# Optimization experiments

Hardware: AMD Instinct MI355X
Metric: run time of the kernel (lower is better)

Reference implementation:

```python
import jax, jax.numpy as jnp
import numpy as np

N_NODES = 100000
N_EDGES = 1000000
D_IN, D_HID, D_OUT = 20, 64, 64
NEG_SLOPE = 0.2


def _gat_layer(x, src, dst, W, a_src, a_dst, b, n_nodes):
    """PyG-style single-head GATConv: message j->i, softmax over incoming edges of i."""
    h = x @ W                                  # [N, D]
    alpha_s = h @ a_src                        # [N]
    alpha_d = h @ a_dst                        # [N]
    e = jax.nn.leaky_relu(alpha_s[src] + alpha_d[dst], NEG_SLOPE)  # [E]
    # numerically-stable segment softmax over destination nodes
    m = jax.ops.segment_max(e, dst, num_segments=n_nodes)          # [N]
    ex = jnp.exp(e - m[dst])                                       # [E]
    denom = jax.ops.segment_sum(ex, dst, num_segments=n_nodes)     # [N]
    alpha = ex / denom[dst]                                        # [E]
    out = jax.ops.segment_sum(alpha[:, None] * h[src], dst, num_segments=n_nodes)
    return out + b


def setup_inputs() -> dict:
    key = jax.random.key(0)
    ks = jax.random.split(key, 11)
    x = jax.random.normal(ks[0], (N_NODES, D_IN), dtype=jnp.float32)
    edge_index = jax.random.randint(ks[1], (2, N_EDGES), 0, N_NODES, dtype=jnp.int64)
    s1 = 1.0 / np.sqrt(D_IN)
    s2 = 1.0 / np.sqrt(D_HID)
    return {
        "x": x,
        "edge_index": edge_index,
        "W1": jax.random.normal(ks[2], (D_IN, D_HID), dtype=jnp.float32) * s1,
        "a_src1": jax.random.normal(ks[3], (D_HID,), dtype=jnp.float32) * s2,
        "a_dst1": jax.random.normal(ks[4], (D_HID,), dtype=jnp.float32) * s2,
        "b1": jnp.zeros((D_HID,), dtype=jnp.float32),
        "W2": jax.random.normal(ks[5], (D_HID, D_OUT), dtype=jnp.float32) * s2,
        "a_src2": jax.random.normal(ks[6], (D_OUT,), dtype=jnp.float32) * s2,
        "a_dst2": jax.random.normal(ks[7], (D_OUT,), dtype=jnp.float32) * s2,
        "b2": jnp.zeros((D_OUT,), dtype=jnp.float32),
    }


def reference(x, edge_index, W1, a_src1, a_dst1, b1, W2, a_src2, a_dst2, b2):
    n = x.shape[0]
    # PyG GATConv adds self-loops by default
    loops = jnp.arange(n, dtype=edge_index.dtype)
    src = jnp.concatenate([edge_index[0], loops])
    dst = jnp.concatenate([edge_index[1], loops])
    h = _gat_layer(x, src, dst, W1, a_src1, a_dst1, b1, n)
    h = jax.nn.relu(h)
    # dropout(p=0.2) is identity in eval mode
    h = _gat_layer(h, src, dst, W2, a_src2, a_dst2, b2, n)
    # global_mean_pool with all-zero batch -> mean over all nodes, shape [1, D_OUT]
    return jnp.mean(h, axis=0, keepdims=True)
```

## Files before the change

### kernel.cpp

```cpp
#include <hip/hip_runtime.h>
#include <math.h>

#define NDIM 64
#define LRELU_SLOPE 0.2f
#define BSHIFT 8
#define BNODES 256
#define ECAP 3584
#define CCAP (ECAP + BNODES)

typedef float f32x2 __attribute__((ext_vector_type(2)));

__device__ __forceinline__ ushort f2bf(float f) {
    unsigned u = __float_as_uint(f);
    unsigned r = (u + 0x7fffu + ((u >> 16) & 1u)) >> 16;
    return (ushort)r;
}
__device__ __forceinline__ float bflo(unsigned u) { return __uint_as_float(u << 16); }
__device__ __forceinline__ float bfhi(unsigned u) { return __uint_as_float(u & 0xffff0000u); }

__global__ void initb_kernel(int* __restrict__ bcur, int nb) {
    int i = blockIdx.x * blockDim.x + threadIdx.x;
    if (i < nb) bcur[i] = i * ECAP;
}

__global__ __launch_bounds__(256) void pg_kernel(
    const int* __restrict__ src, const int* __restrict__ dst,
    int* __restrict__ bcur, unsigned* __restrict__ part, int E, int nb, int PB,
    const float* __restrict__ X, const float* __restrict__ W,
    const float* __restrict__ asrc, const float* __restrict__ adst,
    unsigned char* __restrict__ h, float* __restrict__ as_,
    float* __restrict__ ad_, int N) {
    int t = threadIdx.x;
    if ((int)blockIdx.x < PB) {
        __shared__ int hist[512];
        __shared__ int base[512];
        for (int i = t; i < nb; i += 256) hist[i] = 0;
        __syncthreads();
        int chunk = blockIdx.x * 4096;
        int s[16], d[16];
#pragma unroll
        for (int j = 0; j < 4; ++j) {
            int idx = chunk + j * 1024 + t * 4;
            if (idx + 3 < E) {
                int4 sv = *(const int4*)(src + idx);
                int4 dv = *(const int4*)(dst + idx);
                s[j*4+0]=sv.x; s[j*4+1]=sv.y; s[j*4+2]=sv.z; s[j*4+3]=sv.w;
                d[j*4+0]=dv.x; d[j*4+1]=dv.y; d[j*4+2]=dv.z; d[j*4+3]=dv.w;
            } else {
#pragma unroll
                for (int q = 0; q < 4; ++q) {
                    int i2 = idx + q;
                    if (i2 < E) { s[j*4+q] = src[i2]; d[j*4+q] = dst[i2]; }
                    else        { s[j*4+q] = 0;       d[j*4+q] = -1; }
                }
            }
        }
#pragma unroll
        for (int j = 0; j < 16; ++j)
            if (d[j] >= 0) atomicAdd(&hist[d[j] >> BSHIFT], 1);
        __syncthreads();
        for (int i = t; i < nb; i += 256) {
            int c = hist[i];
            base[i] = c ? atomicAdd(&bcur[i], c) : 0;
            hist[i] = 0;
        }
        __syncthreads();
#pragma unroll
        for (int j = 0; j < 16; ++j) {
            if (d[j] >= 0) {
                int b = d[j] >> BSHIFT;
                int pos = base[b] + atomicAdd(&hist[b], 1);
                int lim = (b + 1) * ECAP - 1;
                if (pos > lim) pos = lim;
                part[pos] = ((unsigned)(d[j] & (BNODES - 1)) << 17) | (unsigned)s[j];
            }
        }
    } else {
        const int K = 20, KS = 32;
        __shared__ float xs[64 * 32];
        __shared__ unsigned hsq[64 * 17];
        __shared__ float ps[2][4][64];
        int base2 = (blockIdx.x - PB) * 64;
        for (int i = t; i < 64 * KS; i += 256) {
            int nl = i / KS, k = i - nl * KS;
            int node = base2 + nl;
            float v = (k < K && node < N) ? X[(size_t)node * K + k] : 0.f;
            xs[nl * KS + ((k + nl) & (KS - 1))] = v;
        }
        __syncthreads();
        int wid = __builtin_amdgcn_readfirstlane(t >> 6);
        int lane = t & 63;
        int node = base2 + lane;
        float acc[16];
#pragma unroll
        for (int j = 0; j < 16; ++j) acc[j] = 0.f;
        const float* Wg = W + wid * 16;
        const float* xrow = xs + lane * KS;
#pragma unroll 4
        for (int k = 0; k < K; ++k) {
            float xk = xrow[(k + lane) & (KS - 1)];
#pragma unroll
            for (int j = 0; j < 16; ++j)
                acc[j] = fmaf(xk, Wg[k * 64 + j], acc[j]);
        }
        float s = 0.f, d = 0.f;
#pragma unroll
        for (int j = 0; j < 16; ++j) {
            s = fmaf(acc[j], asrc[wid * 16 + j], s);
            d = fmaf(acc[j], adst[wid * 16 + j], d);
        }
        ps[0][wid][lane] = s;
        ps[1][wid][lane] = d;
#pragma unroll
        for (int j = 0; j < 16; j += 4) {
            int q = (wid * 16 + j) >> 2;
            int sp = (q + lane) & 15;
            int u = __builtin_amdgcn_cvt_pk_fp8_f32(acc[j], acc[j + 1], 0, false);
            u = __builtin_amdgcn_cvt_pk_fp8_f32(acc[j + 2], acc[j + 3], u, true);
            hsq[lane * 17 + sp] = (unsigned)u;
        }
        __syncthreads();
        if (wid == 0) {
            float s4 = ps[0][0][lane] + ps[0][1][lane] + ps[0][2][lane] + ps[0][3][lane];
            float d4 = ps[1][0][lane] + ps[1][1][lane] + ps[1][2][lane] + ps[1][3][lane];
            if (node < N) { as_[node] = s4; ad_[node] = d4; }
        }
        unsigned* hout = (unsigned*)h;
        for (int pass = 0; pass < 4; ++pass) {
            int row = pass * 16 + (t >> 4);
            int q = t & 15;
            int sp = (q + row) & 15;
            unsigned v = hsq[row * 17 + sp];
            int n2 = base2 + row;
            if (n2 < N) hout[(size_t)n2 * 16 + q] = v;
        }
    }
}

__global__ __launch_bounds__(256) void csr_kernel(
    const int* __restrict__ bcur, const unsigned* __restrict__ part,
    int* __restrict__ csr, int2* __restrict__ offlen, int N) {
    __shared__ int hist[256];
    __shared__ int sc[256];
    int b = blockIdx.x, t = threadIdx.x;
    int nodeBase = b << BSHIFT;
    int nNodes = min(BNODES, N - nodeBase);
    int count = min(bcur[b] - b * ECAP, ECAP);
    hist[t] = (t < nNodes) ? 1 : 0;
    __syncthreads();
    const unsigned* slice = part + (size_t)b * ECAP;
    for (int i = t; i < count; i += 256) {
        int dl = (int)(slice[i] >> 17);
        atomicAdd(&hist[dl], 1);
    }
    __syncthreads();
    int cnt = hist[t];
    sc[t] = cnt;
    __syncthreads();
    for (int o = 1; o < 256; o <<= 1) {
        int v = sc[t];
        int u = (t >= o) ? sc[t - o] : 0;
        __syncthreads();
        sc[t] = v + u;
        __syncthreads();
    }
    int excl = sc[t] - cnt;
    int boff = b * CCAP;
    if (t < nNodes) {
        offlen[nodeBase + t] = make_int2(boff + excl, cnt);
        csr[boff + excl] = nodeBase + t;
    }
    hist[t] = excl + 1;
    __syncthreads();
    for (int i = t; i < count; i += 256) {
        unsigned e = slice[i];
        int dl = (int)(e >> 17);
        int pos = boff + atomicAdd(&hist[dl], 1);
        csr[pos] = (int)(e & 0x1ffffu);
    }
}

template<int K, int KS, bool BF16IN>
__global__ __launch_bounds__(256) void gemm_kernel(
    const void* __restrict__ Xv, const float* __restrict__ W,
    const float* __restrict__ asrc, const float* __restrict__ adst,
    unsigned char* __restrict__ h, float* __restrict__ as_, float* __restrict__ ad_, int N) {
    __shared__ float xs[64 * KS];
    __shared__ unsigned hsq[64 * 17];
    __shared__ float ps[2][4][64];
    int t = threadIdx.x;
    int base = blockIdx.x * 64;
    if (BF16IN) {
        const unsigned* X = (const unsigned*)Xv;
        for (int i = t; i < 64 * (K / 2); i += 256) {
            int nl = i / (K / 2), p = i - nl * (K / 2);
            int k = p * 2;
            int node = base + nl;
            unsigned u = (node < N) ? X[(size_t)node * (K / 2) + p] : 0u;
            xs[nl * KS + ((k + nl) & (KS - 1))] = bflo(u);
            xs[nl * KS + ((k + 1 + nl) & (KS - 1))] = bfhi(u);
        }
    } else {
        const float* X = (const float*)Xv;
        for (int i = t; i < 64 * KS; i += 256) {
            int nl = i / KS, k = i - nl * KS;
            int node = base + nl;
            float v = (k < K && node < N) ? X[(size_t)node * K + k] : 0.f;
            xs[nl * KS + ((k + nl) & (KS - 1))] = v;
        }
    }
    __syncthreads();
    int wid = __builtin_amdgcn_readfirstlane(t >> 6);
    int lane = t & 63;
    int node = base + lane;
    float acc[16];
#pragma unroll
    for (int j = 0; j < 16; ++j) acc[j] = 0.f;
    const float* Wg = W + wid * 16;
    const float* xrow = xs + lane * KS;
#pragma unroll 4
    for (int k = 0; k < K; ++k) {
        float xk = xrow[(k + lane) & (KS - 1)];
#pragma unroll
        for (int j = 0; j < 16; ++j)
            acc[j] = fmaf(xk, Wg[k * 64 + j], acc[j]);
    }
    float s = 0.f, d = 0.f;
#pragma unroll
    for (int j = 0; j < 16; ++j) {
        s = fmaf(acc[j], asrc[wid * 16 + j], s);
        d = fmaf(acc[j], adst[wid * 16 + j], d);
    }
    ps[0][wid][lane] = s;
    ps[1][wid][lane] = d;
#pragma unroll
    for (int j = 0; j < 16; j += 4) {
        int q = (wid * 16 + j) >> 2;
        int sp = (q + lane) & 15;
        int u = __builtin_amdgcn_cvt_pk_fp8_f32(acc[j], acc[j + 1], 0, false);
        u = __builtin_amdgcn_cvt_pk_fp8_f32(acc[j + 2], acc[j + 3], u, true);
        hsq[lane * 17 + sp] = (unsigned)u;
    }
    __syncthreads();
    if (wid == 0) {
        float s4 = ps[0][0][lane] + ps[0][1][lane] + ps[0][2][lane] + ps[0][3][lane];
        float d4 = ps[1][0][lane] + ps[1][1][lane] + ps[1][2][lane] + ps[1][3][lane];
        if (node < N) { as_[node] = s4; ad_[node] = d4; }
    }
    unsigned* hout = (unsigned*)h;
    for (int pass = 0; pass < 4; ++pass) {
        int row = pass * 16 + (t >> 4);
        int q = t & 15;
        int sp = (q + row) & 15;
        unsigned v = hsq[row * 17 + sp];
        int n2 = base + row;
        if (n2 < N) hout[(size_t)n2 * 16 + q] = v;
    }
}

__global__ __launch_bounds__(256) void agg_kernel(
    const int2* __restrict__ offlen, const int* __restrict__ csr,
    const float* __restrict__ as_, const float* __restrict__ ad_,
    const unsigned char* __restrict__ hsrc, const float* __restrict__ bias,
    ushort* __restrict__ out, float* __restrict__ pool, int n, int mode) {
    __shared__ float psum[8][NDIM];
    int wid = threadIdx.x >> 6, lane = threadIdx.x & 63;
    int half = lane >> 5;
    int lh = lane & 31;
    int g = lh >> 3;
    int l = lane & 7;
    int hw = wid * 2 + half;
    int node = blockIdx.x * 8 + hw;
    int base_lane = lane & 32;
    float v[8];
#pragma unroll
    for (int j = 0; j < 8; ++j) v[j] = 0.f;
    if (node < n) {
        int2 ol = offlen[node];
        int off = ol.x, len = ol.y;
        float adi = ad_[node];
        bool vpre = lh < len;
        int skpre = vpre ? csr[off + lh] : 0;
        float apre = vpre ? as_[skpre] : 0.f;
        float tpre = apre + adi;
        tpre = (tpre > 0.f) ? tpre : LRELU_SLOPE * tpre;
        float expre = vpre ? __expf(tpre) : 0.f;
        float den = expre;
        den += __shfl_xor(den, 1);
        den += __shfl_xor(den, 2);
        den += __shfl_xor(den, 4);
        den += __shfl_xor(den, 8);
        den += __shfl_xor(den, 16);
        float acc[8];
#pragma unroll
        for (int j = 0; j < 8; ++j) acc[j] = 0.f;
        if (__all(len <= 32)) {
            uint2 hv[8];
            float exs[8];
#pragma unroll
            for (int c = 0; c < 8; ++c) {
                int e = c * 4 + g;
                int sk = __shfl(skpre, base_lane + e);
                exs[c] = __shfl(expre, base_lane + e);
                const uint2* p = (const uint2*)(hsrc + ((size_t)sk << 6) + (l << 3));
                hv[c] = (e < len) ? *p : make_uint2(0u, 0u);
            }
#pragma unroll
            for (int c = 0; c < 8; ++c) {
                float ex = exs[c];
                f32x2 p0 = __builtin_amdgcn_cvt_pk_f32_fp8(hv[c].x, false);
                f32x2 p1 = __builtin_amdgcn_cvt_pk_f32_fp8(hv[c].x, true);
                f32x2 p2 = __builtin_amdgcn_cvt_pk_f32_fp8(hv[c].y, false);
                f32x2 p3 = __builtin_amdgcn_cvt_pk_f32_fp8(hv[c].y, true);
                acc[0] = fmaf(ex, p0.x, acc[0]);
                acc[1] = fmaf(ex, p0.y, acc[1]);
                acc[2] = fmaf(ex, p1.x, acc[2]);
                acc[3] = fmaf(ex, p1.y, acc[3]);
                acc[4] = fmaf(ex, p2.x, acc[4]);
                acc[5] = fmaf(ex, p2.y, acc[5]);
                acc[6] = fmaf(ex, p3.x, acc[6]);
                acc[7] = fmaf(ex, p3.y, acc[7]);
            }
        } else {
            float den_tail = 0.f;
            int niter = (len + 3) >> 2;
            int sk0 = __shfl(skpre, base_lane + g);
            float ex0 = __shfl(expre, base_lane + g);
            bool ve0 = g < len;
            uint2 hv0 = make_uint2(0, 0);
            if (ve0) hv0 = *(const uint2*)(hsrc + ((size_t)sk0 << 6) + (l << 3));
            int sk1 = __shfl(skpre, base_lane + 4 + g);
            float ex1 = __shfl(expre, base_lane + 4 + g);
            bool ve1 = (4 + g) < len;
            uint2 hv1 = make_uint2(0, 0);
            if (ve1) hv1 = *(const uint2*)(hsrc + ((size_t)sk1 << 6) + (l << 3));
            for (int i = 0; i < niter; ++i) {
                float ex = ex0;
                uint2 hv = hv0;
                ex0 = ex1; hv0 = hv1;
                int e2 = (i + 2) * 4 + g;
                bool ve2 = e2 < len;
                int esrc = e2 < 32 ? e2 : 31;
                sk1 = __shfl(skpre, base_lane + esrc);
                ex1 = __shfl(expre, base_lane + esrc);
                if (e2 >= 32) {
                    if (ve2) {
                        sk1 = csr[off + e2];
                        float a = as_[sk1];
                        float tt = a + adi;
                        tt = (tt > 0.f) ? tt : LRELU_SLOPE * tt;
                        ex1 = __expf(tt);
                        den_tail += ex1;
                    } else ex1 = 0.f;
                }
                hv1 = make_uint2(0, 0);
                if (ve2) hv1 = *(const uint2*)(hsrc + ((size_t)sk1 << 6) + (l << 3));
                f32x2 p0 = __builtin_amdgcn_cvt_pk_f32_fp8(hv.x, false);
                f32x2 p1 = __builtin_amdgcn_cvt_pk_f32_fp8(hv.x, true);
                f32x2 p2 = __builtin_amdgcn_cvt_pk_f32_fp8(hv.y, false);
                f32x2 p3 = __builtin_amdgcn_cvt_pk_f32_fp8(hv.y, true);
                acc[0] = fmaf(ex, p0.x, acc[0]);
                acc[1] = fmaf(ex, p0.y, acc[1]);
                acc[2] = fmaf(ex, p1.x, acc[2]);
                acc[3] = fmaf(ex, p1.y, acc[3]);
                acc[4] = fmaf(ex, p2.x, acc[4]);
                acc[5] = fmaf(ex, p2.y, acc[5]);
                acc[6] = fmaf(ex, p3.x, acc[6]);
                acc[7] = fmaf(ex, p3.y, acc[7]);
            }
            den_tail += __shfl_xor(den_tail, 8);
            den_tail += __shfl_xor(den_tail, 16);
            den += den_tail;
        }
#pragma unroll
        for (int j = 0; j < 8; ++j) {
            acc[j] += __shfl_xor(acc[j], 8);
            acc[j] += __shfl_xor(acc[j], 16);
        }
        float inv = 1.f / den;
        const float4 bv0 = *(const float4*)(bias + l * 8);
        const float4 bv1 = *(const float4*)(bias + l * 8 + 4);
        v[0] = fmaf(acc[0], inv, bv0.x);
        v[1] = fmaf(acc[1], inv, bv0.y);
        v[2] = fmaf(acc[2], inv, bv0.z);
        v[3] = fmaf(acc[3], inv, bv0.w);
        v[4] = fmaf(acc[4], inv, bv1.x);
        v[5] = fmaf(acc[5], inv, bv1.y);
        v[6] = fmaf(acc[6], inv, bv1.z);
        v[7] = fmaf(acc[7], inv, bv1.w);
        if (mode == 1) {
#pragma unroll
            for (int j = 0; j < 8; ++j) v[j] = fmaxf(v[j], 0.f);
            if (g == 0) {
                uint4 pk;
                pk.x = (unsigned)f2bf(v[0]) | ((unsigned)f2bf(v[1]) << 16);
                pk.y = (unsigned)f2bf(v[2]) | ((unsigned)f2bf(v[3]) << 16);
                pk.z = (unsigned)f2bf(v[4]) | ((unsigned)f2bf(v[5]) << 16);
                pk.w = (unsigned)f2bf(v[6]) | ((unsigned)f2bf(v[7]) << 16);
                *(uint4*)(out + (size_t)node * NDIM + l * 8) = pk;
            }
        }
    }
    if (mode == 2) {
        if (g == 0) {
#pragma unroll
            for (int j = 0; j < 8; ++j) psum[hw][l * 8 + j] = v[j];
        }
        __syncthreads();
        if (threadIdx.x < NDIM) {
            float t = 0.f;
#pragma unroll
            for (int r = 0; r < 8; ++r) t += psum[r][threadIdx.x];
            pool[(size_t)blockIdx.x * NDIM + threadIdx.x] = t;
        }
    }
}

__global__ void mean_kernel(const float* __restrict__ pool, float* __restrict__ out,
                            int nb, float invn) {
    __shared__ float sm[4][NDIM];
    int lane = threadIdx.x & 63, wid = threadIdx.x >> 6;
    int row = blockIdx.x * 4 + wid;
    int stride = gridDim.x * 4;
    float s = 0.f;
    for (int i = row; i < nb; i += stride) s += pool[(long)i * NDIM + lane];
    sm[wid][lane] = s;
    __syncthreads();
    if (wid == 0) {
        float v = sm[0][lane] + sm[1][lane] + sm[2][lane] + sm[3][lane];
        atomicAdd(&out[lane], v * invn);
    }
}

extern "C" void kernel_launch(void* const* d_in, const int* in_sizes, int n_in,
                              void* d_out, int out_size, void* d_ws, size_t ws_size,
                              hipStream_t stream) {
    const float* x      = (const float*)d_in[0];
    const int*   eidx   = (const int*)d_in[1];
    const float* W1     = (const float*)d_in[2];
    const float* a_src1 = (const float*)d_in[3];
    const float* a_dst1 = (const float*)d_in[4];
    const float* b1     = (const float*)d_in[5];
    const float* W2     = (const float*)d_in[6];
    const float* a_src2 = (const float*)d_in[7];
    const float* a_dst2 = (const float*)d_in[8];
    const float* b2     = (const float*)d_in[9];
    float* out = (float*)d_out;

    const int N = in_sizes[0] / 20;
    const int E = in_sizes[1] / 2;
    const int* src = eidx;
    const int* dst = eidx + E;
    const int NB = (N + BNODES - 1) >> BSHIFT;

    const int gemm_blocks = (N + 63) / 64;
    const int agg_blocks  = (N + 7) / 8;
    const int PB = (E + 4095) / 4096;

    char* ws = (char*)d_ws;
    unsigned char* h = (unsigned char*)ws;
    ushort* o   = (ushort*)(h + (size_t)N * NDIM);
    float* as_  = (float*)(o + (size_t)N * NDIM);
    float* ad_  = as_ + N;
    int2*  offlen = (int2*)(ad_ + N);
    int*   csr  = (int*)(offlen + N);
    float* pool = (float*)(csr + (size_t)NB * CCAP);
    int*   bcur = (int*)(pool + (size_t)agg_blocks * NDIM);
    unsigned* part = (unsigned*)(bcur + NB);

    hipMemsetAsync(d_out, 0, (size_t)out_size * sizeof(float), stream);

    initb_kernel<<<(NB + 255) / 256, 256, 0, stream>>>(bcur, NB);
    pg_kernel<<<PB + gemm_blocks, 256, 0, stream>>>(
        src, dst, bcur, part, E, NB, PB,
        x, W1, a_src1, a_dst1, h, as_, ad_, N);
    csr_kernel<<<NB, 256, 0, stream>>>(bcur, part, csr, offlen, N);

    agg_kernel<<<agg_blocks, 256, 0, stream>>>(offlen, csr, as_, ad_, h, b1, o, pool, N, 1);

    gemm_kernel<64, 64, true><<<gemm_blocks, 256, 0, stream>>>(o, W2, a_src2, a_dst2, h, as_, ad_, N);
    agg_kernel<<<agg_blocks, 256, 0, stream>>>(offlen, csr, as_, ad_, h, b2, o, pool, N, 2);

    mean_kernel<<<64, 256, 0, stream>>>(pool, out, agg_blocks, 1.0f / (float)N);
}
```

Before: 196.4 us.

## Fuse all GAT stages into one persistent cooperative kernel with grid syncs

Replaces the six separate launches (bucket init, partition plus first GEMM, CSR build, two aggregations, second GEMM, mean) with one persistent cooperative kernel. Each block loops over work units of every stage, and grid-wide barriers separate the stages. Pooling now accumulates per block in shared memory and ends with one atomic per block instead of writing a pool buffer that a separate mean kernel reduces. This removes launch gaps and the pool round-trip, at the cost of grid.sync overhead, a grid capped by occupancy, and register pressure from the union of all stages.

```diff
diff --git a/kernel.cpp b/kernel.cpp
--- a/kernel.cpp
+++ b/kernel.cpp
@@ -1,5 +1,8 @@
 #include <hip/hip_runtime.h>
+#include <hip/hip_cooperative_groups.h>
 #include <math.h>
+
+namespace cg = cooperative_groups;
 
 #define NDIM 64
 #define LRELU_SLOPE 0.2f
@@ -18,178 +21,69 @@
 __device__ __forceinline__ float bflo(unsigned u) { return __uint_as_float(u << 16); }
 __device__ __forceinline__ float bfhi(unsigned u) { return __uint_as_float(u & 0xffff0000u); }
 
-__global__ void initb_kernel(int* __restrict__ bcur, int nb) {
-    int i = blockIdx.x * blockDim.x + threadIdx.x;
-    if (i < nb) bcur[i] = i * ECAP;
-}
-
-__global__ __launch_bounds__(256) void pg_kernel(
+#define SMEM_BYTES 22784
+
+__device__ __forceinline__ void part_unit(
+    unsigned char* SMEM, int unit,
     const int* __restrict__ src, const int* __restrict__ dst,
-    int* __restrict__ bcur, unsigned* __restrict__ part, int E, int nb, int PB,
-    const float* __restrict__ X, const float* __restrict__ W,
+    int* __restrict__ bcur, unsigned* __restrict__ part, int E, int nb) {
+    int* hist = (int*)SMEM;
+    int* base = (int*)(SMEM + 2048);
+    int t = threadIdx.x;
+    for (int i = t; i < nb; i += 256) hist[i] = 0;
+    __syncthreads();
+    int chunk = unit * 4096;
+    int s[16], d[16];
+#pragma unroll
+    for (int j = 0; j < 4; ++j) {
+        int idx = chunk + j * 1024 + t * 4;
+        if (idx + 3 < E) {
+            int4 sv = *(const int4*)(src + idx);
+            int4 dv = *(const int4*)(dst + idx);
+            s[j*4+0]=sv.x; s[j*4+1]=sv.y; s[j*4+2]=sv.z; s[j*4+3]=sv.w;
+            d[j*4+0]=dv.x; d[j*4+1]=dv.y; d[j*4+2]=dv.z; d[j*4+3]=dv.w;
+        } else {
+#pragma unroll
+            for (int q = 0; q < 4; ++q) {
+                int i2 = idx + q;
+                if (i2 < E) { s[j*4+q] = src[i2]; d[j*4+q] = dst[i2]; }
+                else        { s[j*4+q] = 0;       d[j*4+q] = -1; }
+            }
+        }
+    }
+#pragma unroll
+    for (int j = 0; j < 16; ++j)
+        if (d[j] >= 0) atomicAdd(&hist[d[j] >> BSHIFT], 1);
+    __syncthreads();
+    for (int i = t; i < nb; i += 256) {
+        int c = hist[i];
+        base[i] = c ? atomicAdd(&bcur[i], c) : 0;
+        hist[i] = 0;
+    }
+    __syncthreads();
+#pragma unroll
+    for (int j = 0; j < 16; ++j) {
+        if (d[j] >= 0) {
+            int b = d[j] >> BSHIFT;
+            int pos = base[b] + atomicAdd(&hist[b], 1);
+            int lim = (b + 1) * ECAP - 1;
+            if (pos > lim) pos = lim;
+            part[pos] = ((unsigned)(d[j] & (BNODES - 1)) << 17) | (unsigned)s[j];
+        }
+    }
+}
+
+template<int K, int KS, bool BF16IN>
+__device__ __forceinline__ void gemm_unit(
+    unsigned char* SMEM, int base,
+    const void* __restrict__ Xv, const float* __restrict__ W,
     const float* __restrict__ asrc, const float* __restrict__ adst,
     unsigned char* __restrict__ h, float* __restrict__ as_,
     float* __restrict__ ad_, int N) {
+    float* xs = (float*)SMEM;
+    unsigned* hsq = (unsigned*)(SMEM + 16384);
+    auto ps = (float(*)[4][64])(SMEM + 20736);
     int t = threadIdx.x;
-    if ((int)blockIdx.x < PB) {
-        __shared__ int hist[512];
-        __shared__ int base[512];
-        for (int i = t; i < nb; i += 256) hist[i] = 0;
-        __syncthreads();
-        int chunk = blockIdx.x * 4096;
-        int s[16], d[16];
-#pragma unroll
-        for (int j = 0; j < 4; ++j) {
-            int idx = chunk + j * 1024 + t * 4;
-            if (idx + 3 < E) {
-                int4 sv = *(const int4*)(src + idx);
-                int4 dv = *(const int4*)(dst + idx);
-                s[j*4+0]=sv.x; s[j*4+1]=sv.y; s[j*4+2]=sv.z; s[j*4+3]=sv.w;
-                d[j*4+0]=dv.x; d[j*4+1]=dv.y; d[j*4+2]=dv.z; d[j*4+3]=dv.w;
-            } else {
-#pragma unroll
-                for (int q = 0; q < 4; ++q) {
-                    int i2 = idx + q;
-                    if (i2 < E) { s[j*4+q] = src[i2]; d[j*4+q] = dst[i2]; }
-                    else        { s[j*4+q] = 0;       d[j*4+q] = -1; }
-                }
-            }
-        }
-#pragma unroll
-        for (int j = 0; j < 16; ++j)
-            if (d[j] >= 0) atomicAdd(&hist[d[j] >> BSHIFT], 1);
-        __syncthreads();
-        for (int i = t; i < nb; i += 256) {
-            int c = hist[i];
-            base[i] = c ? atomicAdd(&bcur[i], c) : 0;
-            hist[i] = 0;
-        }
-        __syncthreads();
-#pragma unroll
-        for (int j = 0; j < 16; ++j) {
-            if (d[j] >= 0) {
-                int b = d[j] >> BSHIFT;
-                int pos = base[b] + atomicAdd(&hist[b], 1);
-                int lim = (b + 1) * ECAP - 1;
-                if (pos > lim) pos = lim;
-                part[pos] = ((unsigned)(d[j] & (BNODES - 1)) << 17) | (unsigned)s[j];
-            }
-        }
-    } else {
-        const int K = 20, KS = 32;
-        __shared__ float xs[64 * 32];
-        __shared__ unsigned hsq[64 * 17];
-        __shared__ float ps[2][4][64];
-        int base2 = (blockIdx.x - PB) * 64;
-        for (int i = t; i < 64 * KS; i += 256) {
-            int nl = i / KS, k = i - nl * KS;
-            int node = base2 + nl;
-            float v = (k < K && node < N) ? X[(size_t)node * K + k] : 0.f;
-            xs[nl * KS + ((k + nl) & (KS - 1))] = v;
-        }
-        __syncthreads();
-        int wid = __builtin_amdgcn_readfirstlane(t >> 6);
-        int lane = t & 63;
-        int node = base2 + lane;
-        float acc[16];
-#pragma unroll
-        for (int j = 0; j < 16; ++j) acc[j] = 0.f;
-        const float* Wg = W + wid * 16;
-        const float* xrow = xs + lane * KS;
-#pragma unroll 4
-        for (int k = 0; k < K; ++k) {
-            float xk = xrow[(k + lane) & (KS - 1)];
-#pragma unroll
-            for (int j = 0; j < 16; ++j)
-                acc[j] = fmaf(xk, Wg[k * 64 + j], acc[j]);
-        }
-        float s = 0.f, d = 0.f;
-#pragma unroll
-        for (int j = 0; j < 16; ++j) {
-            s = fmaf(acc[j], asrc[wid * 16 + j], s);
-            d = fmaf(acc[j], adst[wid * 16 + j], d);
-        }
-        ps[0][wid][lane] = s;
-        ps[1][wid][lane] = d;
-#pragma unroll
-        for (int j = 0; j < 16; j += 4) {
-            int q = (wid * 16 + j) >> 2;
-            int sp = (q + lane) & 15;
-            int u = __builtin_amdgcn_cvt_pk_fp8_f32(acc[j], acc[j + 1], 0, false);
-            u = __builtin_amdgcn_cvt_pk_fp8_f32(acc[j + 2], acc[j + 3], u, true);
-            hsq[lane * 17 + sp] = (unsigned)u;
-        }
-        __syncthreads();
-        if (wid == 0) {
-            float s4 = ps[0][0][lane] + ps[0][1][lane] + ps[0][2][lane] + ps[0][3][lane];
-            float d4 = ps[1][0][lane] + ps[1][1][lane] + ps[1][2][lane] + ps[1][3][lane];
-            if (node < N) { as_[node] = s4; ad_[node] = d4; }
-        }
-        unsigned* hout = (unsigned*)h;
-        for (int pass = 0; pass < 4; ++pass) {
-            int row = pass * 16 + (t >> 4);
-            int q = t & 15;
-            int sp = (q + row) & 15;
-            unsigned v = hsq[row * 17 + sp];
-            int n2 = base2 + row;
-            if (n2 < N) hout[(size_t)n2 * 16 + q] = v;
-        }
-    }
-}
-
-__global__ __launch_bounds__(256) void csr_kernel(
-    const int* __restrict__ bcur, const unsigned* __restrict__ part,
-    int* __restrict__ csr, int2* __restrict__ offlen, int N) {
-    __shared__ int hist[256];
-    __shared__ int sc[256];
-    int b = blockIdx.x, t = threadIdx.x;
-    int nodeBase = b << BSHIFT;
-    int nNodes = min(BNODES, N - nodeBase);
-    int count = min(bcur[b] - b * ECAP, ECAP);
-    hist[t] = (t < nNodes) ? 1 : 0;
-    __syncthreads();
-    const unsigned* slice = part + (size_t)b * ECAP;
-    for (int i = t; i < count; i += 256) {
-        int dl = (int)(slice[i] >> 17);
-        atomicAdd(&hist[dl], 1);
-    }
-    __syncthreads();
-    int cnt = hist[t];
-    sc[t] = cnt;
-    __syncthreads();
-    for (int o = 1; o < 256; o <<= 1) {
-        int v = sc[t];
-        int u = (t >= o) ? sc[t - o] : 0;
-        __syncthreads();
-        sc[t] = v + u;
-        __syncthreads();
-    }
-    int excl = sc[t] - cnt;
-    int boff = b * CCAP;
-    if (t < nNodes) {
-        offlen[nodeBase + t] = make_int2(boff + excl, cnt);
-        csr[boff + excl] = nodeBase + t;
-    }
-    hist[t] = excl + 1;
-    __syncthreads();
-    for (int i = t; i < count; i += 256) {
-        unsigned e = slice[i];
-        int dl = (int)(e >> 17);
-        int pos = boff + atomicAdd(&hist[dl], 1);
-        csr[pos] = (int)(e & 0x1ffffu);
-    }
-}
-
-template<int K, int KS, bool BF16IN>
-__global__ __launch_bounds__(256) void gemm_kernel(
-    const void* __restrict__ Xv, const float* __restrict__ W,
-    const float* __restrict__ asrc, const float* __restrict__ adst,
-    unsigned char* __restrict__ h, float* __restrict__ as_, float* __restrict__ ad_, int N) {
-    __shared__ float xs[64 * KS];
-    __shared__ unsigned hsq[64 * 17];
-    __shared__ float ps[2][4][64];
-    int t = threadIdx.x;
-    int base = blockIdx.x * 64;
     if (BF16IN) {
         const unsigned* X = (const unsigned*)Xv;
         for (int i = t; i < 64 * (K / 2); i += 256) {
@@ -258,19 +152,64 @@
     }
 }
 
-__global__ __launch_bounds__(256) void agg_kernel(
+__device__ __forceinline__ void csr_unit(
+    unsigned char* SMEM, int b,
+    const int* __restrict__ bcur, const unsigned* __restrict__ part,
+    int* __restrict__ csr, int2* __restrict__ offlen, int N) {
+    int* hist = (int*)SMEM;
+    int* sc = (int*)(SMEM + 1024);
+    int t = threadIdx.x;
+    int nodeBase = b << BSHIFT;
+    int nNodes = min(BNODES, N - nodeBase);
+    int count = min(bcur[b] - b * ECAP, ECAP);
+    hist[t] = (t < nNodes) ? 1 : 0;
+    __syncthreads();
+    const unsigned* slice = part + (size_t)b * ECAP;
+    for (int i = t; i < count; i += 256) {
+        int dl = (int)(slice[i] >> 17);
+        atomicAdd(&hist[dl], 1);
+    }
+    __syncthreads();
+    int cnt = hist[t];
+    sc[t] = cnt;
+    __syncthreads();
+    for (int o = 1; o < 256; o <<= 1) {
+        int v = sc[t];
+        int u = (t >= o) ? sc[t - o] : 0;
+        __syncthreads();
+        sc[t] = v + u;
+        __syncthreads();
+    }
+    int excl = sc[t] - cnt;
+    int boff = b * CCAP;
+    if (t < nNodes) {
+        offlen[nodeBase + t] = make_int2(boff + excl, cnt);
+        csr[boff + excl] = nodeBase + t;
+    }
+    hist[t] = excl + 1;
+    __syncthreads();
+    for (int i = t; i < count; i += 256) {
+        unsigned e = slice[i];
+        int dl = (int)(e >> 17);
+        int pos = boff + atomicAdd(&hist[dl], 1);
+        csr[pos] = (int)(e & 0x1ffffu);
+    }
+}
+
+template<int MODE>
+__device__ __forceinline__ void agg_unit(
+    unsigned char* SMEM, int unit,
     const int2* __restrict__ offlen, const int* __restrict__ csr,
     const float* __restrict__ as_, const float* __restrict__ ad_,
     const unsigned char* __restrict__ hsrc, const float* __restrict__ bias,
-    ushort* __restrict__ out, float* __restrict__ pool, int n, int mode) {
-    __shared__ float psum[8][NDIM];
+    ushort* __restrict__ out_, float* __restrict__ bacc, int n) {
     int wid = threadIdx.x >> 6, lane = threadIdx.x & 63;
     int half = lane >> 5;
     int lh = lane & 31;
     int g = lh >> 3;
     int l = lane & 7;
     int hw = wid * 2 + half;
-    int node = blockIdx.x * 8 + hw;
+    int node = unit * 8 + hw;
     int base_lane = lane & 32;
     float v[8];
 #pragma unroll
@@ -388,7 +327,7 @@
         v[5] = fmaf(acc[5], inv, bv1.y);
         v[6] = fmaf(acc[6], inv, bv1.z);
         v[7] = fmaf(acc[7], inv, bv1.w);
-        if (mode == 1) {
+        if (MODE == 1) {
 #pragma unroll
             for (int j = 0; j < 8; ++j) v[j] = fmaxf(v[j], 0.f);
             if (g == 0) {
@@ -397,38 +336,80 @@
                 pk.y = (unsigned)f2bf(v[2]) | ((unsigned)f2bf(v[3]) << 16);
                 pk.z = (unsigned)f2bf(v[4]) | ((unsigned)f2bf(v[5]) << 16);
                 pk.w = (unsigned)f2bf(v[6]) | ((unsigned)f2bf(v[7]) << 16);
-                *(uint4*)(out + (size_t)node * NDIM + l * 8) = pk;
+                *(uint4*)(out_ + (size_t)node * NDIM + l * 8) = pk;
             }
         }
     }
-    if (mode == 2) {
+    if (MODE == 2) {
+        auto psum = (float(*)[NDIM])SMEM;
         if (g == 0) {
 #pragma unroll
             for (int j = 0; j < 8; ++j) psum[hw][l * 8 + j] = v[j];
         }
         __syncthreads();
         if (threadIdx.x < NDIM) {
-            float t = 0.f;
-#pragma unroll
-            for (int r = 0; r < 8; ++r) t += psum[r][threadIdx.x];
-            pool[(size_t)blockIdx.x * NDIM + threadIdx.x] = t;
-        }
-    }
-}
-
-__global__ void mean_kernel(const float* __restrict__ pool, float* __restrict__ out,
-                            int nb, float invn) {
-    __shared__ float sm[4][NDIM];
-    int lane = threadIdx.x & 63, wid = threadIdx.x >> 6;
-    int row = blockIdx.x * 4 + wid;
-    int stride = gridDim.x * 4;
-    float s = 0.f;
-    for (int i = row; i < nb; i += stride) s += pool[(long)i * NDIM + lane];
-    sm[wid][lane] = s;
-    __syncthreads();
-    if (wid == 0) {
-        float v = sm[0][lane] + sm[1][lane] + sm[2][lane] + sm[3][lane];
-        atomicAdd(&out[lane], v * invn);
+            float s = 0.f;
+#pragma unroll
+            for (int r = 0; r < 8; ++r) s += psum[r][threadIdx.x];
+            bacc[threadIdx.x] += s;
+        }
+        __syncthreads();
+    }
+}
+
+__global__ __launch_bounds__(256, 4) void giga_kernel(
+    const int* __restrict__ src, const int* __restrict__ dst,
+    int* __restrict__ bcur, unsigned* __restrict__ part,
+    int E, int nb, int PB, int GB, int AU,
+    const float* __restrict__ x,
+    const float* __restrict__ W1, const float* __restrict__ as1v,
+    const float* __restrict__ ad1v, const float* __restrict__ b1,
+    const float* __restrict__ W2, const float* __restrict__ as2v,
+    const float* __restrict__ ad2v, const float* __restrict__ b2,
+    unsigned char* __restrict__ h, ushort* __restrict__ o,
+    float* __restrict__ as_, float* __restrict__ ad_,
+    int2* __restrict__ offlen, int* __restrict__ csr,
+    float* __restrict__ out, int N, float invn) {
+    __shared__ __align__(16) unsigned char SMEM[SMEM_BYTES];
+    cg::grid_group grid = cg::this_grid();
+    int t = threadIdx.x;
+    int G = gridDim.x;
+
+    for (int i = blockIdx.x * 256 + t; i < nb; i += G * 256) bcur[i] = i * ECAP;
+    grid.sync();
+
+    for (int u = blockIdx.x; u < PB + GB; u += G) {
+        if (u < PB) part_unit(SMEM, u, src, dst, bcur, part, E, nb);
+        else gemm_unit<20, 32, false>(SMEM, (u - PB) * 64, x, W1, as1v, ad1v, h, as_, ad_, N);
+        __syncthreads();
+    }
+    grid.sync();
+
+    for (int u = blockIdx.x; u < nb; u += G) {
+        csr_unit(SMEM, u, bcur, part, csr, offlen, N);
+        __syncthreads();
+    }
+    grid.sync();
+
+    for (int u = blockIdx.x; u < AU; u += G)
+        agg_unit<1>(SMEM, u, offlen, csr, as_, ad_, h, b1, o, nullptr, N);
+    grid.sync();
+
+    for (int u = blockIdx.x; u < GB; u += G) {
+        gemm_unit<64, 64, true>(SMEM, u * 64, o, W2, as2v, ad2v, h, as_, ad_, N);
+        __syncthreads();
+    }
+    grid.sync();
+
+    float* bacc = (float*)(SMEM + 2048);
+    if (t < NDIM) bacc[t] = 0.f;
+    __syncthreads();
+    for (int u = blockIdx.x; u < AU; u += G)
+        agg_unit<2>(SMEM, u, offlen, csr, as_, ad_, h, b2, o, bacc, N);
+    if (t < NDIM) {
+        float s = bacc[t];
+        if (s != 0.f) atomicAdd(&out[t], s * invn);
+        else atomicAdd(&out[t], s * invn);
     }
 }
 
@@ -452,9 +433,8 @@
     const int* src = eidx;
     const int* dst = eidx + E;
     const int NB = (N + BNODES - 1) >> BSHIFT;
-
-    const int gemm_blocks = (N + 63) / 64;
-    const int agg_blocks  = (N + 7) / 8;
+    const int GB = (N + 63) / 64;
+    const int AU = (N + 7) / 8;
     const int PB = (E + 4095) / 4096;
 
     char* ws = (char*)d_ws;
@@ -464,22 +444,28 @@
     float* ad_  = as_ + N;
     int2*  offlen = (int2*)(ad_ + N);
     int*   csr  = (int*)(offlen + N);
-    float* pool = (float*)(csr + (size_t)NB * CCAP);
-    int*   bcur = (int*)(pool + (size_t)agg_blocks * NDIM);
+    int*   bcur = (int*)(csr + (size_t)NB * CCAP);
     unsigned* part = (unsigned*)(bcur + NB);
 
     hipMemsetAsync(d_out, 0, (size_t)out_size * sizeof(float), stream);
 
-    initb_kernel<<<(NB + 255) / 256, 256, 0, stream>>>(bcur, NB);
-    pg_kernel<<<PB + gemm_blocks, 256, 0, stream>>>(
-        src, dst, bcur, part, E, NB, PB,
-        x, W1, a_src1, a_dst1, h, as_, ad_, N);
-    csr_kernel<<<NB, 256, 0, stream>>>(bcur, part, csr, offlen, N);
-
-    agg_kernel<<<agg_blocks, 256, 0, stream>>>(offlen, csr, as_, ad_, h, b1, o, pool, N, 1);
-
-    gemm_kernel<64, 64, true><<<gemm_blocks, 256, 0, stream>>>(o, W2, a_src2, a_dst2, h, as_, ad_, N);
-    agg_kernel<<<agg_blocks, 256, 0, stream>>>(offlen, csr, as_, ad_, h, b2, o, pool, N, 2);
-
-    mean_kernel<<<64, 256, 0, stream>>>(pool, out, agg_blocks, 1.0f / (float)N);
-}
+    int bpc = 0;
+    hipOccupancyMaxActiveBlocksPerMultiprocessor(&bpc, giga_kernel, 256, 0);
+    if (bpc < 1) bpc = 1;
+    int G = bpc * 256;
+    if (G > 2048) G = 2048;
+
+    float invn = 1.0f / (float)N;
+    void* args[] = {
+        (void*)&src, (void*)&dst, (void*)&bcur, (void*)&part,
+        (void*)&E, (void*)&NB, (void*)&PB, (void*)&GB, (void*)&AU,
+        (void*)&x,
+        (void*)&W1, (void*)&a_src1, (void*)&a_dst1, (void*)&b1,
+        (void*)&W2, (void*)&a_src2, (void*)&a_dst2, (void*)&b2,
+        (void*)&h, (void*)&o, (void*)&as_, (void*)&ad_,
+        (void*)&offlen, (void*)&csr,
+        (void*)&out, (void*)&N, (void*)&invn,
+    };
+    hipLaunchCooperativeKernel((const void*)giga_kernel, dim3(G), dim3(256),
+                               args, 0, stream);
+}
```

Measured after the change: 553.1 us. 2.82x slower.

## Fold layer-2 GEMM through aggregation by linearity and pool before projecting

Applied to the files above, without the earlier changes.

The layer-2 feature transform is removed. Layer-2 attention logits are computed in agg1 as dot products of the layer-1 output with W2·a_src2 and W2·a_dst2, precomputed in csr_kernel. Layer-2 aggregation then runs over the bf16 64-dim layer-1 output, and W2 is applied only once after mean pooling, with b2 added at the end. Separately, the partition chunk per block is halved and bucket counters become relative offsets cleared by a memset, which removes the init kernel. The trade-off is that the layer-2 gather now reads 128-byte bf16 rows instead of 64-byte fp8 rows.

```diff
diff --git a/kernel.cpp b/kernel.cpp
--- a/kernel.cpp
+++ b/kernel.cpp
@@ -17,11 +17,6 @@
 }
 __device__ __forceinline__ float bflo(unsigned u) { return __uint_as_float(u << 16); }
 __device__ __forceinline__ float bfhi(unsigned u) { return __uint_as_float(u & 0xffff0000u); }
-
-__global__ void initb_kernel(int* __restrict__ bcur, int nb) {
-    int i = blockIdx.x * blockDim.x + threadIdx.x;
-    if (i < nb) bcur[i] = i * ECAP;
-}
 
 __global__ __launch_bounds__(256) void pg_kernel(
     const int* __restrict__ src, const int* __restrict__ dst,
@@ -36,10 +31,10 @@
         __shared__ int base[512];
         for (int i = t; i < nb; i += 256) hist[i] = 0;
         __syncthreads();
-        int chunk = blockIdx.x * 4096;
-        int s[16], d[16];
-#pragma unroll
-        for (int j = 0; j < 4; ++j) {
+        int chunk = blockIdx.x * 2048;
+        int s[8], d[8];
+#pragma unroll
+        for (int j = 0; j < 2; ++j) {
             int idx = chunk + j * 1024 + t * 4;
             if (idx + 3 < E) {
                 int4 sv = *(const int4*)(src + idx);
@@ -56,7 +51,7 @@
             }
         }
 #pragma unroll
-        for (int j = 0; j < 16; ++j)
+        for (int j = 0; j < 8; ++j)
             if (d[j] >= 0) atomicAdd(&hist[d[j] >> BSHIFT], 1);
         __syncthreads();
         for (int i = t; i < nb; i += 256) {
@@ -66,13 +61,13 @@
         }
         __syncthreads();
 #pragma unroll
-        for (int j = 0; j < 16; ++j) {
+        for (int j = 0; j < 8; ++j) {
             if (d[j] >= 0) {
                 int b = d[j] >> BSHIFT;
-                int pos = base[b] + atomicAdd(&hist[b], 1);
-                int lim = (b + 1) * ECAP - 1;
-                if (pos > lim) pos = lim;
-                part[pos] = ((unsigned)(d[j] & (BNODES - 1)) << 17) | (unsigned)s[j];
+                int loc = base[b] + atomicAdd(&hist[b], 1);
+                if (loc > ECAP - 1) loc = ECAP - 1;
+                part[(size_t)b * ECAP + loc] =
+                    ((unsigned)(d[j] & (BNODES - 1)) << 17) | (unsigned)s[j];
             }
         }
     } else {
@@ -139,13 +134,15 @@
 
 __global__ __launch_bounds__(256) void csr_kernel(
     const int* __restrict__ bcur, const unsigned* __restrict__ part,
-    int* __restrict__ csr, int2* __restrict__ offlen, int N) {
+    int* __restrict__ csr, int2* __restrict__ offlen, int N,
+    const float* __restrict__ W2, const float* __restrict__ a_src2,
+    const float* __restrict__ a_dst2, float* __restrict__ atil) {
     __shared__ int hist[256];
     __shared__ int sc[256];
     int b = blockIdx.x, t = threadIdx.x;
     int nodeBase = b << BSHIFT;
     int nNodes = min(BNODES, N - nodeBase);
-    int count = min(bcur[b] - b * ECAP, ECAP);
+    int count = min(bcur[b], ECAP);
     hist[t] = (t < nNodes) ? 1 : 0;
     __syncthreads();
     const unsigned* slice = part + (size_t)b * ECAP;
@@ -178,92 +175,24 @@
         int pos = boff + atomicAdd(&hist[dl], 1);
         csr[pos] = (int)(e & 0x1ffffu);
     }
-}
-
-template<int K, int KS, bool BF16IN>
-__global__ __launch_bounds__(256) void gemm_kernel(
-    const void* __restrict__ Xv, const float* __restrict__ W,
-    const float* __restrict__ asrc, const float* __restrict__ adst,
-    unsigned char* __restrict__ h, float* __restrict__ as_, float* __restrict__ ad_, int N) {
-    __shared__ float xs[64 * KS];
-    __shared__ unsigned hsq[64 * 17];
-    __shared__ float ps[2][4][64];
-    int t = threadIdx.x;
-    int base = blockIdx.x * 64;
-    if (BF16IN) {
-        const unsigned* X = (const unsigned*)Xv;
-        for (int i = t; i < 64 * (K / 2); i += 256) {
-            int nl = i / (K / 2), p = i - nl * (K / 2);
-            int k = p * 2;
-            int node = base + nl;
-            unsigned u = (node < N) ? X[(size_t)node * (K / 2) + p] : 0u;
-            xs[nl * KS + ((k + nl) & (KS - 1))] = bflo(u);
-            xs[nl * KS + ((k + 1 + nl) & (KS - 1))] = bfhi(u);
-        }
-    } else {
-        const float* X = (const float*)Xv;
-        for (int i = t; i < 64 * KS; i += 256) {
-            int nl = i / KS, k = i - nl * KS;
-            int node = base + nl;
-            float v = (k < K && node < N) ? X[(size_t)node * K + k] : 0.f;
-            xs[nl * KS + ((k + nl) & (KS - 1))] = v;
-        }
-    }
-    __syncthreads();
-    int wid = __builtin_amdgcn_readfirstlane(t >> 6);
-    int lane = t & 63;
-    int node = base + lane;
-    float acc[16];
-#pragma unroll
-    for (int j = 0; j < 16; ++j) acc[j] = 0.f;
-    const float* Wg = W + wid * 16;
-    const float* xrow = xs + lane * KS;
-#pragma unroll 4
-    for (int k = 0; k < K; ++k) {
-        float xk = xrow[(k + lane) & (KS - 1)];
-#pragma unroll
-        for (int j = 0; j < 16; ++j)
-            acc[j] = fmaf(xk, Wg[k * 64 + j], acc[j]);
-    }
-    float s = 0.f, d = 0.f;
-#pragma unroll
-    for (int j = 0; j < 16; ++j) {
-        s = fmaf(acc[j], asrc[wid * 16 + j], s);
-        d = fmaf(acc[j], adst[wid * 16 + j], d);
-    }
-    ps[0][wid][lane] = s;
-    ps[1][wid][lane] = d;
-#pragma unroll
-    for (int j = 0; j < 16; j += 4) {
-        int q = (wid * 16 + j) >> 2;
-        int sp = (q + lane) & 15;
-        int u = __builtin_amdgcn_cvt_pk_fp8_f32(acc[j], acc[j + 1], 0, false);
-        u = __builtin_amdgcn_cvt_pk_fp8_f32(acc[j + 2], acc[j + 3], u, true);
-        hsq[lane * 17 + sp] = (unsigned)u;
-    }
-    __syncthreads();
-    if (wid == 0) {
-        float s4 = ps[0][0][lane] + ps[0][1][lane] + ps[0][2][lane] + ps[0][3][lane];
-        float d4 = ps[1][0][lane] + ps[1][1][lane] + ps[1][2][lane] + ps[1][3][lane];
-        if (node < N) { as_[node] = s4; ad_[node] = d4; }
-    }
-    unsigned* hout = (unsigned*)h;
-    for (int pass = 0; pass < 4; ++pass) {
-        int row = pass * 16 + (t >> 4);
-        int q = t & 15;
-        int sp = (q + row) & 15;
-        unsigned v = hsq[row * 17 + sp];
-        int n2 = base + row;
-        if (n2 < N) hout[(size_t)n2 * 16 + q] = v;
-    }
-}
-
-__global__ __launch_bounds__(256) void agg_kernel(
+    if (b == 0 && t < 128) {
+        int j = t & 63;
+        const float* av = (t < 64) ? a_src2 : a_dst2;
+        const float* wr = W2 + (size_t)j * 64;
+        float s = 0.f;
+#pragma unroll 8
+        for (int k = 0; k < 64; ++k) s = fmaf(wr[k], av[k], s);
+        atil[t] = s;
+    }
+}
+
+__global__ __launch_bounds__(256) void agg1_kernel(
     const int2* __restrict__ offlen, const int* __restrict__ csr,
     const float* __restrict__ as_, const float* __restrict__ ad_,
     const unsigned char* __restrict__ hsrc, const float* __restrict__ bias,
-    ushort* __restrict__ out, float* __restrict__ pool, int n, int mode) {
-    __shared__ float psum[8][NDIM];
+    const float* __restrict__ atil,
+    ushort* __restrict__ out, float* __restrict__ as2,
+    float* __restrict__ ad2, int n) {
     int wid = threadIdx.x >> 6, lane = threadIdx.x & 63;
     int half = lane >> 5;
     int lh = lane & 31;
@@ -272,9 +201,6 @@
     int hw = wid * 2 + half;
     int node = blockIdx.x * 8 + hw;
     int base_lane = lane & 32;
-    float v[8];
-#pragma unroll
-    for (int j = 0; j < 8; ++j) v[j] = 0.f;
     if (node < n) {
         int2 ol = offlen[node];
         int off = ol.x, len = ol.y;
@@ -380,45 +306,170 @@
         float inv = 1.f / den;
         const float4 bv0 = *(const float4*)(bias + l * 8);
         const float4 bv1 = *(const float4*)(bias + l * 8 + 4);
-        v[0] = fmaf(acc[0], inv, bv0.x);
-        v[1] = fmaf(acc[1], inv, bv0.y);
-        v[2] = fmaf(acc[2], inv, bv0.z);
-        v[3] = fmaf(acc[3], inv, bv0.w);
-        v[4] = fmaf(acc[4], inv, bv1.x);
-        v[5] = fmaf(acc[5], inv, bv1.y);
-        v[6] = fmaf(acc[6], inv, bv1.z);
-        v[7] = fmaf(acc[7], inv, bv1.w);
-        if (mode == 1) {
-#pragma unroll
-            for (int j = 0; j < 8; ++j) v[j] = fmaxf(v[j], 0.f);
-            if (g == 0) {
-                uint4 pk;
-                pk.x = (unsigned)f2bf(v[0]) | ((unsigned)f2bf(v[1]) << 16);
-                pk.y = (unsigned)f2bf(v[2]) | ((unsigned)f2bf(v[3]) << 16);
-                pk.z = (unsigned)f2bf(v[4]) | ((unsigned)f2bf(v[5]) << 16);
-                pk.w = (unsigned)f2bf(v[6]) | ((unsigned)f2bf(v[7]) << 16);
-                *(uint4*)(out + (size_t)node * NDIM + l * 8) = pk;
-            }
-        }
-    }
-    if (mode == 2) {
+        float v[8];
+        v[0] = fmaxf(fmaf(acc[0], inv, bv0.x), 0.f);
+        v[1] = fmaxf(fmaf(acc[1], inv, bv0.y), 0.f);
+        v[2] = fmaxf(fmaf(acc[2], inv, bv0.z), 0.f);
+        v[3] = fmaxf(fmaf(acc[3], inv, bv0.w), 0.f);
+        v[4] = fmaxf(fmaf(acc[4], inv, bv1.x), 0.f);
+        v[5] = fmaxf(fmaf(acc[5], inv, bv1.y), 0.f);
+        v[6] = fmaxf(fmaf(acc[6], inv, bv1.z), 0.f);
+        v[7] = fmaxf(fmaf(acc[7], inv, bv1.w), 0.f);
         if (g == 0) {
-#pragma unroll
-            for (int j = 0; j < 8; ++j) psum[hw][l * 8 + j] = v[j];
-        }
-        __syncthreads();
-        if (threadIdx.x < NDIM) {
-            float t = 0.f;
-#pragma unroll
-            for (int r = 0; r < 8; ++r) t += psum[r][threadIdx.x];
-            pool[(size_t)blockIdx.x * NDIM + threadIdx.x] = t;
-        }
-    }
-}
-
-__global__ void mean_kernel(const float* __restrict__ pool, float* __restrict__ out,
-                            int nb, float invn) {
+            uint4 pk;
+            pk.x = (unsigned)f2bf(v[0]) | ((unsigned)f2bf(v[1]) << 16);
+            pk.y = (unsigned)f2bf(v[2]) | ((unsigned)f2bf(v[3]) << 16);
+            pk.z = (unsigned)f2bf(v[4]) | ((unsigned)f2bf(v[5]) << 16);
+            pk.w = (unsigned)f2bf(v[6]) | ((unsigned)f2bf(v[7]) << 16);
+            *(uint4*)(out + (size_t)node * NDIM + l * 8) = pk;
+        }
+        const float4 s0 = *(const float4*)(atil + l * 8);
+        const float4 s1 = *(const float4*)(atil + l * 8 + 4);
+        const float4 d0 = *(const float4*)(atil + 64 + l * 8);
+        const float4 d1 = *(const float4*)(atil + 64 + l * 8 + 4);
+        float sp = v[0]*s0.x + v[1]*s0.y + v[2]*s0.z + v[3]*s0.w
+                 + v[4]*s1.x + v[5]*s1.y + v[6]*s1.z + v[7]*s1.w;
+        float dp = v[0]*d0.x + v[1]*d0.y + v[2]*d0.z + v[3]*d0.w
+                 + v[4]*d1.x + v[5]*d1.y + v[6]*d1.z + v[7]*d1.w;
+        sp += __shfl_xor(sp, 1); sp += __shfl_xor(sp, 2); sp += __shfl_xor(sp, 4);
+        dp += __shfl_xor(dp, 1); dp += __shfl_xor(dp, 2); dp += __shfl_xor(dp, 4);
+        if (lh == 0) { as2[node] = sp; ad2[node] = dp; }
+    }
+}
+
+__global__ __launch_bounds__(256) void agg2_kernel(
+    const int2* __restrict__ offlen, const int* __restrict__ csr,
+    const float* __restrict__ as_, const float* __restrict__ ad_,
+    const ushort* __restrict__ osrc, float* __restrict__ pool, int n) {
+    __shared__ float psum[8][NDIM];
+    int wid = threadIdx.x >> 6, lane = threadIdx.x & 63;
+    int half = lane >> 5;
+    int lh = lane & 31;
+    int g = lh >> 3;
+    int l = lane & 7;
+    int hw = wid * 2 + half;
+    int node = blockIdx.x * 8 + hw;
+    int base_lane = lane & 32;
+    float v[8];
+#pragma unroll
+    for (int j = 0; j < 8; ++j) v[j] = 0.f;
+    if (node < n) {
+        int2 ol = offlen[node];
+        int off = ol.x, len = ol.y;
+        float adi = ad_[node];
+        bool vpre = lh < len;
+        int skpre = vpre ? csr[off + lh] : 0;
+        float apre = vpre ? as_[skpre] : 0.f;
+        float tpre = apre + adi;
+        tpre = (tpre > 0.f) ? tpre : LRELU_SLOPE * tpre;
+        float expre = vpre ? __expf(tpre) : 0.f;
+        float den = expre;
+        den += __shfl_xor(den, 1);
+        den += __shfl_xor(den, 2);
+        den += __shfl_xor(den, 4);
+        den += __shfl_xor(den, 8);
+        den += __shfl_xor(den, 16);
+        float acc[8];
+#pragma unroll
+        for (int j = 0; j < 8; ++j) acc[j] = 0.f;
+        if (__all(len <= 32)) {
+            uint4 hv[8];
+            float exs[8];
+#pragma unroll
+            for (int c = 0; c < 8; ++c) {
+                int e = c * 4 + g;
+                int sk = __shfl(skpre, base_lane + e);
+                exs[c] = __shfl(expre, base_lane + e);
+                const uint4* p = (const uint4*)(osrc + ((size_t)sk << 6) + (l << 3));
+                hv[c] = (e < len) ? *p : make_uint4(0u, 0u, 0u, 0u);
+            }
+#pragma unroll
+            for (int c = 0; c < 8; ++c) {
+                float ex = exs[c];
+                acc[0] = fmaf(ex, bflo(hv[c].x), acc[0]);
+                acc[1] = fmaf(ex, bfhi(hv[c].x), acc[1]);
+                acc[2] = fmaf(ex, bflo(hv[c].y), acc[2]);
+                acc[3] = fmaf(ex, bfhi(hv[c].y), acc[3]);
+                acc[4] = fmaf(ex, bflo(hv[c].z), acc[4]);
+                acc[5] = fmaf(ex, bfhi(hv[c].z), acc[5]);
+                acc[6] = fmaf(ex, bflo(hv[c].w), acc[6]);
+                acc[7] = fmaf(ex, bfhi(hv[c].w), acc[7]);
+            }
+        } else {
+            float den_tail = 0.f;
+            int niter = (len + 3) >> 2;
+            int sk0 = __shfl(skpre, base_lane + g);
+            float ex0 = __shfl(expre, base_lane + g);
+            bool ve0 = g < len;
+            uint4 hv0 = make_uint4(0, 0, 0, 0);
+            if (ve0) hv0 = *(const uint4*)(osrc + ((size_t)sk0 << 6) + (l << 3));
+            int sk1 = __shfl(skpre, base_lane + 4 + g);
+            float ex1 = __shfl(expre, base_lane + 4 + g);
+            bool ve1 = (4 + g) < len;
+            uint4 hv1 = make_uint4(0, 0, 0, 0);
+            if (ve1) hv1 = *(const uint4*)(osrc + ((size_t)sk1 << 6) + (l << 3));
+            for (int i = 0; i < niter; ++i) {
+                float ex = ex0;
+                uint4 hv = hv0;
+                ex0 = ex1; hv0 = hv1;
+                int e2 = (i + 2) * 4 + g;
+                bool ve2 = e2 < len;
+                int esrc = e2 < 32 ? e2 : 31;
+                sk1 = __shfl(skpre, base_lane + esrc);
+                ex1 = __shfl(expre, base_lane + esrc);
+                if (e2 >= 32) {
+                    if (ve2) {
+                        sk1 = csr[off + e2];
+                        float a = as_[sk1];
+                        float tt = a + adi;
+                        tt = (tt > 0.f) ? tt : LRELU_SLOPE * tt;
+                        ex1 = __expf(tt);
+                        den_tail += ex1;
+                    } else ex1 = 0.f;
+                }
+                hv1 = make_uint4(0, 0, 0, 0);
+                if (ve2) hv1 = *(const uint4*)(osrc + ((size_t)sk1 << 6) + (l << 3));
+                acc[0] = fmaf(ex, bflo(hv.x), acc[0]);
+                acc[1] = fmaf(ex, bfhi(hv.x), acc[1]);
+                acc[2] = fmaf(ex, bflo(hv.y), acc[2]);
+                acc[3] = fmaf(ex, bfhi(hv.y), acc[3]);
+                acc[4] = fmaf(ex, bflo(hv.z), acc[4]);
+                acc[5] = fmaf(ex, bfhi(hv.z), acc[5]);
+                acc[6] = fmaf(ex, bflo(hv.w), acc[6]);
+                acc[7] = fmaf(ex, bfhi(hv.w), acc[7]);
+            }
+            den_tail += __shfl_xor(den_tail, 8);
+            den_tail += __shfl_xor(den_tail, 16);
+            den += den_tail;
+        }
+#pragma unroll
+        for (int j = 0; j < 8; ++j) {
+            acc[j] += __shfl_xor(acc[j], 8);
+            acc[j] += __shfl_xor(acc[j], 16);
+        }
+        float inv = 1.f / den;
+#pragma unroll
+        for (int j = 0; j < 8; ++j) v[j] = acc[j] * inv;
+    }
+    if (g == 0) {
+#pragma unroll
+        for (int j = 0; j < 8; ++j) psum[hw][l * 8 + j] = v[j];
+    }
+    __syncthreads();
+    if (threadIdx.x < NDIM) {
+        float t = 0.f;
+#pragma unroll
+        for (int r = 0; r < 8; ++r) t += psum[r][threadIdx.x];
+        pool[(size_t)blockIdx.x * NDIM + threadIdx.x] = t;
+    }
+}
+
+__global__ void mean_kernel(const float* __restrict__ pool,
+                            const float* __restrict__ W2,
+                            const float* __restrict__ b2,
+                            float* __restrict__ out, int nb, float invn) {
     __shared__ float sm[4][NDIM];
+    __shared__ float zs[NDIM];
     int lane = threadIdx.x & 63, wid = threadIdx.x >> 6;
     int row = blockIdx.x * 4 + wid;
     int stride = gridDim.x * 4;
@@ -427,8 +478,16 @@
     sm[wid][lane] = s;
     __syncthreads();
     if (wid == 0) {
-        float v = sm[0][lane] + sm[1][lane] + sm[2][lane] + sm[3][lane];
-        atomicAdd(&out[lane], v * invn);
+        zs[lane] = sm[0][lane] + sm[1][lane] + sm[2][lane] + sm[3][lane];
+    }
+    __syncthreads();
+    if (wid == 0) {
+        float y = 0.f;
+#pragma unroll 8
+        for (int j = 0; j < 64; ++j)
+            y = fmaf(zs[j], W2[(size_t)j * 64 + lane], y);
+        atomicAdd(&out[lane], y * invn);
+        if (blockIdx.x == 0) atomicAdd(&out[lane], b2[lane]);
     }
 }
 
@@ -455,31 +514,37 @@
 
     const int gemm_blocks = (N + 63) / 64;
     const int agg_blocks  = (N + 7) / 8;
-    const int PB = (E + 4095) / 4096;
+    const int PB = (E + 2047) / 2048;
 
     char* ws = (char*)d_ws;
     unsigned char* h = (unsigned char*)ws;
     ushort* o   = (ushort*)(h + (size_t)N * NDIM);
-    float* as_  = (float*)(o + (size_t)N * NDIM);
-    float* ad_  = as_ + N;
-    int2*  offlen = (int2*)(ad_ + N);
+    float* as1  = (float*)(o + (size_t)N * NDIM);
+    float* ad1  = as1 + N;
+    float* as2  = ad1 + N;
+    float* ad2  = as2 + N;
+    int2*  offlen = (int2*)(ad2 + N);
     int*   csr  = (int*)(offlen + N);
     float* pool = (float*)(csr + (size_t)NB * CCAP);
-    int*   bcur = (int*)(pool + (size_t)agg_blocks * NDIM);
+    float* atil = pool + (size_t)agg_blocks * NDIM;
+    int*   bcur = (int*)(atil + 128);
     unsigned* part = (unsigned*)(bcur + NB);
 
     hipMemsetAsync(d_out, 0, (size_t)out_size * sizeof(float), stream);
-
-    initb_kernel<<<(NB + 255) / 256, 256, 0, stream>>>(bcur, NB);
+    hipMemsetAsync(bcur, 0, (size_t)NB * sizeof(int), stream);
+
     pg_kernel<<<PB + gemm_blocks, 256, 0, stream>>>(
         src, dst, bcur, part, E, NB, PB,
-        x, W1, a_src1, a_dst1, h, as_, ad_, N);
-    csr_kernel<<<NB, 256, 0, stream>>>(bcur, part, csr, offlen, N);
-
-    agg_kernel<<<agg_blocks, 256, 0, stream>>>(offlen, csr, as_, ad_, h, b1, o, pool, N, 1);
-
-    gemm_kernel<64, 64, true><<<gemm_blocks, 256, 0, stream>>>(o, W2, a_src2, a_dst2, h, as_, ad_, N);
-    agg_kernel<<<agg_blocks, 256, 0, stream>>>(offlen, csr, as_, ad_, h, b2, o, pool, N, 2);
-
-    mean_kernel<<<64, 256, 0, stream>>>(pool, out, agg_blocks, 1.0f / (float)N);
-}
+        x, W1, a_src1, a_dst1, h, as1, ad1, N);
+    csr_kernel<<<NB, 256, 0, stream>>>(bcur, part, csr, offlen, N,
+                                       W2, a_src2, a_dst2, atil);
+
+    agg1_kernel<<<agg_blocks, 256, 0, stream>>>(
+        offlen, csr, as1, ad1, h, b1, atil, o, as2, ad2, N);
+
+    agg2_kernel<<<agg_blocks, 256, 0, stream>>>(
+        offlen, csr, as2, ad2, o, pool, N);
+
+    mean_kernel<<<64, 256, 0, stream>>>(pool, W2, b2, out, agg_blocks,
+                                        1.0f / (float)N);
+}
```

Result: no change. 193.8 us (-1.3%).
